# Kernel optimization log

Hardware: AMD Instinct MI355X
Metric: run time of the kernel (lower is better)

The kernel has to match this reference:

```python
import jax, jax.numpy as jnp
import numpy as np

B, C, H, W, NH = 8, 256, 32, 32, 4  # batch, channels, height, width, heads


def groupnorm(x, w, b, eps=1e-5):
    # GroupNorm with 1 group: normalize over (C,H,W) per sample
    mu = x.mean(axis=(1, 2, 3), keepdims=True)
    var = x.var(axis=(1, 2, 3), keepdims=True)
    xn = (x - mu) * jax.lax.rsqrt(var + eps)
    return xn * w[None, :, None, None] + b[None, :, None, None]


def setup_inputs() -> dict:
    key = jax.random.key(0)
    ks = jax.random.split(key, 6)
    C4 = 4 * C
    s = lambda k, shape, scale: jax.random.normal(k, shape, jnp.float32) * scale
    return {
        "x": jax.random.normal(ks[0], (B, C, H, W), jnp.float32),
        "qkv_w": s(ks[1], (3 * C, C), 0.05),   # 1x1 conv, no bias
        "uh_w": s(ks[2], (C, C), 0.05),
        "uh_b": jnp.zeros((C,), jnp.float32),
        "n1_w": jnp.ones((C,), jnp.float32),
        "n1_b": jnp.zeros((C,), jnp.float32),
        "n2_w": jnp.ones((C,), jnp.float32),
        "n2_b": jnp.zeros((C,), jnp.float32),
        "f1_w": s(ks[3], (C4, C), 0.05),
        "f1_b": jnp.zeros((C4,), jnp.float32),
        "f2_w": s(ks[4], (C, C4), 0.05),
        "f2_b": jnp.zeros((C,), jnp.float32),
        # torch inits these to 0; use nonzero values so both branches contribute
        "gamma_attn": jnp.array(0.5, jnp.float32),
        "gamma_ffn": jnp.array(0.5, jnp.float32),
    }


def reference(x, qkv_w, uh_w, uh_b, n1_w, n1_b, n2_w, n2_b,
              f1_w, f1_b, f2_w, f2_b, gamma_attn, gamma_ffn):
    Bx, Cx, Hx, Wx = x.shape
    N = Hx * Wx
    dk = Cx // NH
    # --- attention branch (eval mode: DropPath is identity) ---
    xn = groupnorm(x, n1_w, n1_b).reshape(Bx, Cx, N)
    qkv = jnp.einsum('oc,bcn->bon', qkv_w, xn)          # 1x1 conv == channel matmul
    q, k, v = [t.reshape(Bx, NH, dk, N) for t in jnp.split(qkv, 3, axis=1)]
    scores = jnp.einsum('bhdi,bhdj->bhij', q, k) / np.float32(np.sqrt(dk))
    attn = jax.nn.softmax(scores, axis=-1)               # [B,H,N,N]
    out = jnp.einsum('bhij,bhdj->bhdi', attn, v).reshape(Bx, Cx, N)
    uh = jnp.einsum('oc,bcn->bon', uh_w, out) + uh_b[None, :, None]
    x2 = x + gamma_attn * uh.reshape(Bx, Cx, Hx, Wx)
    # --- FFN branch ---
    h = groupnorm(x2, n2_w, n2_b).reshape(Bx, Cx, N)
    h = jax.nn.silu(jnp.einsum('oc,bcn->bon', f1_w, h) + f1_b[None, :, None])
    h = jnp.einsum('oc,bcn->bon', f2_w, h) + f2_b[None, :, None]
    return x2 + gamma_ffn * h.reshape(Bx, Cx, Hx, Wx)
```

## Files before the change

### kernel.cpp

```cpp
#include <hip/hip_runtime.h>
#include <math.h>

#define Bsz 8
#define Cch 256
#define Nsp 1024
#define NHd 4
#define QS  0.18033688011112042f

using bf16x8  = __attribute__((ext_vector_type(8))) short;
using f32x4   = __attribute__((ext_vector_type(4))) float;
using ushort8 = __attribute__((ext_vector_type(8))) unsigned short;
#define MFMA(a,b,c) __builtin_amdgcn_mfma_f32_16x16x32_bf16(a,b,c,0,0,0)

__device__ inline unsigned short f2bf(float f) {
    unsigned int u = __float_as_uint(f);
    u = u + 0x7fffu + ((u >> 16) & 1u);
    return (unsigned short)(u >> 16);
}
__device__ inline float bf2f(unsigned short u) {
    return __uint_as_float((unsigned int)u << 16);
}
__device__ inline unsigned int cvtpk(float lo, float hi) {
    unsigned int r;
    asm("v_cvt_pk_bf16_f32 %0, %1, %2" : "=v"(r) : "v"(lo), "v"(hi));
    return r;
}

__global__ __launch_bounds__(256) void wconv_gn(const float* __restrict__ a, const float* __restrict__ b,
                                                const float* __restrict__ c, const float* __restrict__ d,
                                                unsigned short* __restrict__ o,
                                                const float* __restrict__ x,
                                                float* __restrict__ part) {
    if (blockIdx.x < 3072) {
        size_t i = (size_t)blockIdx.x * 256 + threadIdx.x;
        float v;
        if (i < 196608) v = a[i];
        else if (i < 262144) v = b[i - 196608];
        else if (i < 524288) v = c[i - 262144];
        else v = d[i - 524288];
        o[i] = f2bf(v);
        return;
    }
    int blk = blockIdx.x - 3072;
    int bb = blk >> 6;
    const float* xb = x + (size_t)bb * (Cch * Nsp) + (size_t)(blk & 63) * 4096;
    int t = threadIdx.x;
    float s = 0.f, s2 = 0.f;
    for (int i = t; i < 4096; i += 256) { float v = xb[i]; s += v; s2 += v * v; }
    __shared__ float sh[256], sh2[256];
    sh[t] = s; sh2[t] = s2; __syncthreads();
    for (int off = 128; off; off >>= 1) {
        if (t < off) { sh[t] += sh[t + off]; sh2[t] += sh2[t + off]; }
        __syncthreads();
    }
    if (t == 0) { part[blk * 2] = sh[0]; part[blk * 2 + 1] = sh2[0]; }
}

template<int K, int KL, int NFRAG>
__global__ __launch_bounds__(256, 4) void gemm_lds(
        const unsigned short* __restrict__ W,
        const unsigned short* __restrict__ Xcl,
        int epi, int act, int xmode,
        unsigned short* __restrict__ ocl, int Ocl, int ocol0,
        unsigned short* __restrict__ orm,
        float* __restrict__ pf, const float* __restrict__ res,
        unsigned short* __restrict__ x2cl,
        const float* __restrict__ gamma, const float* __restrict__ bias,
        float* __restrict__ part,
        const float* __restrict__ gnpart,
        const float* __restrict__ gnw, const float* __restrict__ gnb) {
    static_assert(KL == 256 && K == 256, "single-round K only");
    constexpr int NTILE = NFRAG * 16;
    constexpr int CPR = KL / 8;
    constexpr int TOTCH = NTILE * CPR;
    int b = blockIdx.z, nb = blockIdx.x, ob = blockIdx.y;
    int t = threadIdx.x, w = t >> 6, l = t & 63, lg = l >> 4, lm = l & 15;
    __shared__ unsigned short Xs[NTILE * KL];
    __shared__ float sgn[2];
    const unsigned short* Xb = Xcl + ((size_t)b * Nsp + nb * NTILE) * K;
    int o_base = ob * 256 + w * 64;
    const unsigned short* Wp = W + (size_t)(o_base + lm) * K + 8 * lg;
    int m8 = lm & 15 & 7;

    bf16x8 wr[3][4];
    #define WLOAD(sl, g_) do {                                             \
        const unsigned short* wp_ = Wp + ((g_) & 7) * 32;                  \
        wr[sl][0] = *(const bf16x8*)(wp_);                                 \
        wr[sl][1] = *(const bf16x8*)(wp_ + (size_t)16 * K);                \
        wr[sl][2] = *(const bf16x8*)(wp_ + (size_t)32 * K);                \
        wr[sl][3] = *(const bf16x8*)(wp_ + (size_t)48 * K);                \
    } while (0)
    WLOAD(0, 0);
    WLOAD(1, 1);

    if (xmode == 0) {
        #pragma unroll
        for (int i = 0; i < TOTCH / 256; i++) {
            int c = i * 256 + t;
            int n = c / CPR, s = c % CPR;
            int gc = s ^ (n & 7);
            *(bf16x8*)&Xs[c * 8] = *(const bf16x8*)(Xb + (size_t)n * K + gc * 8);
        }
    } else if (xmode == 1) {
        if (t < 64) {
            float s = gnpart[(b * 64 + t) * 2], s2 = gnpart[(b * 64 + t) * 2 + 1];
            for (int m = 1; m < 64; m <<= 1) { s += __shfl_xor(s, m); s2 += __shfl_xor(s2, m); }
            if (t == 0) {
                float inv_n = 1.f / (Cch * Nsp);
                float mu = s * inv_n;
                float var = s2 * inv_n - mu * mu;
                sgn[0] = mu; sgn[1] = rsqrtf(var + 1e-5f);
            }
        }
        __syncthreads();
        float mu = sgn[0], rs = sgn[1];
        #pragma unroll
        for (int i = 0; i < TOTCH / 256; i++) {
            int c = i * 256 + t;
            int n = c / CPR, s = c % CPR;
            int gc = s ^ (n & 7);
            ushort8 xv = *(const ushort8*)(Xb + (size_t)n * K + gc * 8);
            f32x4 w0 = *(const f32x4*)(gnw + gc * 8);
            f32x4 w1 = *(const f32x4*)(gnw + gc * 8 + 4);
            f32x4 b0 = *(const f32x4*)(gnb + gc * 8);
            f32x4 b1 = *(const f32x4*)(gnb + gc * 8 + 4);
            ushort8 rr;
            #pragma unroll
            for (int j = 0; j < 4; j++) {
                rr[j]     = f2bf((bf2f(xv[j])     - mu) * rs * w0[j] + b0[j]);
                rr[4 + j] = f2bf((bf2f(xv[4 + j]) - mu) * rs * w1[j] + b1[j]);
            }
            *(ushort8*)&Xs[c * 8] = rr;
        }
    } else if (xmode == 2) {
        const size_t SPO = (size_t)Bsz * Nsp * Cch;
        #pragma unroll
        for (int i = 0; i < TOTCH / 256; i++) {
            int c = i * 256 + t;
            int n = c / CPR, s = c % CPR;
            int gc = s ^ (n & 7);
            const unsigned short* p0 = Xb + (size_t)n * K + gc * 8;
            int h = gc >> 3;
            int gn = nb * NTILE + n;
            float a0[8] = {};
            float lsum = 0.f;
            #pragma unroll
            for (int sp = 0; sp < 4; sp++) {
                ushort8 ov = *(const ushort8*)(p0 + (size_t)sp * SPO);
                #pragma unroll
                for (int j = 0; j < 8; j++) a0[j] += bf2f(ov[j]);
                lsum += gnpart[(((size_t)sp * Bsz + b) * NHd + h) * Nsp + gn];
            }
            float inv = 1.f / lsum;
            ushort8 rr;
            #pragma unroll
            for (int j = 0; j < 8; j++) rr[j] = f2bf(a0[j] * inv);
            *(ushort8*)&Xs[c * 8] = rr;
        }
    } else {
        if (t < 64) {
            float s = gnpart[(b * 64 + t) * 2], s2 = gnpart[(b * 64 + t) * 2 + 1];
            for (int m = 1; m < 64; m <<= 1) { s += __shfl_xor(s, m); s2 += __shfl_xor(s2, m); }
            if (t == 0) {
                float inv_n = 1.f / (Cch * Nsp);
                float mu = s * inv_n;
                float var = s2 * inv_n - mu * mu;
                sgn[0] = mu; sgn[1] = rsqrtf(var + 1e-5f);
            }
        }
        __syncthreads();
        float mu = sgn[0], rs = sgn[1];
        int n = t & 31;
        #pragma unroll
        for (int i = 0; i < 4; i++) {
            int G = i * 8 + (t >> 5);
            const float* xr = res + ((size_t)b * Cch + G * 8) * Nsp + (size_t)nb * NTILE + n;
            ushort8 rr;
            #pragma unroll
            for (int j = 0; j < 8; j++) {
                float val = xr[(size_t)j * Nsp];
                rr[j] = f2bf((val - mu) * rs * gnw[G * 8 + j] + gnb[G * 8 + j]);
            }
            int slot = G ^ (n & 7);
            *(ushort8*)&Xs[(n * 32 + slot) * 8] = rr;
        }
    }
    __syncthreads();

    f32x4 acc[4][NFRAG] = {};
    #define KSTEP(sl, s_) do {                                             \
        _Pragma("unroll")                                                  \
        for (int nf = 0; nf < NFRAG; nf++) {                               \
            int slot = ((s_) * 4 + lg) ^ m8;                               \
            bf16x8 xf = *(const bf16x8*)&Xs[((nf * 16 + lm) * CPR + slot) * 8]; \
            acc[0][nf] = MFMA(wr[sl][0], xf, acc[0][nf]);                  \
            acc[1][nf] = MFMA(wr[sl][1], xf, acc[1][nf]);                  \
            acc[2][nf] = MFMA(wr[sl][2], xf, acc[2][nf]);                  \
            acc[3][nf] = MFMA(wr[sl][3], xf, acc[3][nf]);                  \
        }                                                                  \
    } while (0)
    #pragma unroll
    for (int s = 0; s < 8; s++) {
        if (s < 6) WLOAD((s + 2) % 3, s + 2);
        KSTEP(s % 3, s);
    }
    #undef WLOAD
    #undef KSTEP

    if (epi == 0) {
        if (act == 3 && o_base >= 512) {
            #pragma unroll
            for (int nf = 0; nf < NFRAG; nf++) {
                int n = nb * NTILE + nf * 16 + lm;
                #pragma unroll
                for (int q = 0; q < 4; q++)
                    #pragma unroll
                    for (int r = 0; r < 4; r++) {
                        int o = o_base + q * 16 + 4 * lg + r - 512;
                        orm[((size_t)b * Cch + o) * Nsp + n] = f2bf(acc[q][nf][r]);
                    }
            }
        } else {
            float sc = (act == 3 && o_base < 256) ? QS : 1.f;
            #pragma unroll
            for (int nf = 0; nf < NFRAG; nf++) {
                int n = nb * NTILE + nf * 16 + lm;
                unsigned short* dst = ocl + ((size_t)b * Nsp + n) * Ocl + ocol0 + o_base + 4 * lg;
                #pragma unroll
                for (int q = 0; q < 4; q++) {
                    unsigned long long pk = 0;
                    #pragma unroll
                    for (int r = 0; r < 4; r++) {
                        int o = o_base + q * 16 + 4 * lg + r;
                        float v = acc[q][nf][r];
                        if (bias) v += bias[o];
                        if (act == 1) v = v / (1.f + __expf(-v));
                        else v *= sc;
                        pk |= (unsigned long long)f2bf(v) << (16 * r);
                    }
                    *(unsigned long long*)(dst + q * 16) = pk;
                }
            }
        }
    } else {
        float g = gamma[0];
        float ps = 0.f, ps2 = 0.f;
        #pragma unroll
        for (int nf = 0; nf < NFRAG; nf++) {
            int n = nb * NTILE + nf * 16 + lm;
            unsigned short* cdst = x2cl + ((size_t)b * Nsp + n) * Cch + o_base + 4 * lg;
            #pragma unroll
            for (int q = 0; q < 4; q++) {
                unsigned long long pk = 0;
                #pragma unroll
                for (int r = 0; r < 4; r++) {
                    int o = o_base + q * 16 + 4 * lg + r;
                    float v = acc[q][nf][r];
                    if (bias) v += bias[o];
                    size_t idx = ((size_t)b * Cch + o) * Nsp + n;
                    float ov = res[idx] + g * v;
                    pf[idx] = ov;
                    ps += ov; ps2 += ov * ov;
                    pk |= (unsigned long long)f2bf(ov) << (16 * r);
                }
                *(unsigned long long*)(cdst + q * 16) = pk;
            }
        }
        float* rsh  = (float*)&Xs[0];
        float* rsh2 = rsh + 256;
        __syncthreads();
        rsh[t] = ps; rsh2[t] = ps2; __syncthreads();
        for (int off = 128; off; off >>= 1) {
            if (t < off) { rsh[t] += rsh[t + off]; rsh2[t] += rsh2[t + off]; }
            __syncthreads();
        }
        if (t == 0) {
            int slot = b * gridDim.x + nb;
            part[slot * 2] = rsh[0]; part[slot * 2 + 1] = rsh2[0];
        }
    }
}

__global__ __launch_bounds__(256, 2) void ffn_fused(
        const unsigned short* __restrict__ Wf1,
        const unsigned short* __restrict__ Wf2,
        const unsigned short* __restrict__ x2cl,
        const float* __restrict__ gnpart,
        const float* __restrict__ gnw, const float* __restrict__ gnb,
        const float* __restrict__ f1b, const float* __restrict__ f2b,
        const float* __restrict__ gamma,
        const float* __restrict__ x2, float* __restrict__ out) {
    int b = blockIdx.z, nb = blockIdx.x;
    int t = threadIdx.x, w = t >> 6, l = t & 63, lg = l >> 4, lm = l & 15;
    __shared__ unsigned short Xs[32 * 256];
    __shared__ unsigned short H[4][32 * 256];
    __shared__ float sgn[2];
    const unsigned short* Xb = x2cl + ((size_t)b * Nsp + nb * 32) * 256;
    int m8 = lm & 7;

    bf16x8 wr[3][4];
    const unsigned short* Wp;
    #define WLOADF(sl, g_, KK) do {                                        \
        const unsigned short* wp_ = Wp + ((g_) >> 3) * 256 + ((g_) & 7) * 32; \
        wr[sl][0] = *(const bf16x8*)(wp_);                                 \
        wr[sl][1] = *(const bf16x8*)(wp_ + (size_t)16 * (KK));             \
        wr[sl][2] = *(const bf16x8*)(wp_ + (size_t)32 * (KK));             \
        wr[sl][3] = *(const bf16x8*)(wp_ + (size_t)48 * (KK));             \
    } while (0)

    if (t < 64) {
        float s = gnpart[(b * 64 + t) * 2], s2 = gnpart[(b * 64 + t) * 2 + 1];
        for (int m = 1; m < 64; m <<= 1) { s += __shfl_xor(s, m); s2 += __shfl_xor(s2, m); }
        if (t == 0) {
            float inv_n = 1.f / (Cch * Nsp);
            float mu = s * inv_n;
            float var = s2 * inv_n - mu * mu;
            sgn[0] = mu; sgn[1] = rsqrtf(var + 1e-5f);
        }
    }
    Wp = Wf1 + (size_t)(w * 64 + lm) * 256 + 8 * lg;
    WLOADF(0, 0, 256);
    WLOADF(1, 1, 256);
    __syncthreads();
    {
        float mu = sgn[0], rs = sgn[1];
        #pragma unroll
        for (int i = 0; i < 4; i++) {
            int c = i * 256 + t;
            int n = c / 32, s = c % 32;
            int gc = s ^ (n & 7);
            ushort8 xv = *(const ushort8*)(Xb + (size_t)n * 256 + gc * 8);
            f32x4 w0 = *(const f32x4*)(gnw + gc * 8);
            f32x4 w1 = *(const f32x4*)(gnw + gc * 8 + 4);
            f32x4 b0 = *(const f32x4*)(gnb + gc * 8);
            f32x4 b1 = *(const f32x4*)(gnb + gc * 8 + 4);
            ushort8 rr;
            #pragma unroll
            for (int j = 0; j < 4; j++) {
                rr[j]     = f2bf((bf2f(xv[j])     - mu) * rs * w0[j] + b0[j]);
                rr[4 + j] = f2bf((bf2f(xv[4 + j]) - mu) * rs * w1[j] + b1[j]);
            }
            *(ushort8*)&Xs[c * 8] = rr;
        }
    }
    __syncthreads();

    f32x4 acc[4][2];
    #define KSTEPF(sl, s_, Xp) do {                                        \
        _Pragma("unroll")                                                  \
        for (int nf = 0; nf < 2; nf++) {                                   \
            int slot = ((s_) * 4 + lg) ^ m8;                               \
            bf16x8 xf = *(const bf16x8*)&(Xp)[((nf * 16 + lm) * 32 + slot) * 8]; \
            acc[0][nf] = MFMA(wr[sl][0], xf, acc[0][nf]);                  \
            acc[1][nf] = MFMA(wr[sl][1], xf, acc[1][nf]);                  \
            acc[2][nf] = MFMA(wr[sl][2], xf, acc[2][nf]);                  \
            acc[3][nf] = MFMA(wr[sl][3], xf, acc[3][nf]);                  \
        }                                                                  \
    } while (0)
    #define F1PASS(obp, NEXTPROLOG) do {                                   \
        _Pragma("unroll")                                                  \
        for (int q = 0; q < 4; q++)                                        \
            _Pragma("unroll")                                              \
            for (int nf = 0; nf < 2; nf++) acc[q][nf] = (f32x4){0.f, 0.f, 0.f, 0.f}; \
        _Pragma("unroll")                                                  \
        for (int s = 0; s < 8; s++) {                                      \
            if (s < 6) WLOADF((s + 2) % 3, s + 2, 256);                    \
            KSTEPF(s % 3, s, Xs);                                          \
        }                                                                  \
        NEXTPROLOG;                                                        \
        _Pragma("unroll")                                                  \
        for (int nf = 0; nf < 2; nf++) {                                   \
            int n = nf * 16 + lm;                                          \
            _Pragma("unroll")                                              \
            for (int q = 0; q < 4; q++) {                                  \
                unsigned long long pk = 0;                                 \
                _Pragma("unroll")                                          \
                for (int r = 0; r < 4; r++) {                              \
                    int oin = w * 64 + q * 16 + 4 * lg + r;                \
                    float v = acc[q][nf][r] + f1b[(obp) * 256 + oin];      \
                    v = v / (1.f + __expf(-v));                            \
                    pk |= (unsigned long long)f2bf(v) << (16 * r);         \
                }                                                          \
                int G = w * 8 + q * 2 + (lg >> 1);                         \
                int slot = G ^ (n & 7);                                    \
                *(unsigned long long*)&H[obp][(n * 32 + slot) * 8 + 4 * (lg & 1)] = pk; \
            }                                                              \
        }                                                                  \
    } while (0)

    F1PASS(0, { Wp = Wf1 + (size_t)(256 + w * 64 + lm) * 256 + 8 * lg;
                WLOADF(0, 0, 256); WLOADF(1, 1, 256); });
    F1PASS(1, { Wp = Wf1 + (size_t)(512 + w * 64 + lm) * 256 + 8 * lg;
                WLOADF(0, 0, 256); WLOADF(1, 1, 256); });
    F1PASS(2, { Wp = Wf1 + (size_t)(768 + w * 64 + lm) * 256 + 8 * lg;
                WLOADF(0, 0, 256); WLOADF(1, 1, 256); });
    F1PASS(3, { Wp = Wf2 + (size_t)(w * 64 + lm) * 1024 + 8 * lg;
                WLOADF(0, 0, 1024); WLOADF(1, 1, 1024); });
    __syncthreads();

    #pragma unroll
    for (int q = 0; q < 4; q++)
        #pragma unroll
        for (int nf = 0; nf < 2; nf++) acc[q][nf] = (f32x4){0.f, 0.f, 0.f, 0.f};
    #pragma unroll
    for (int g = 0; g < 32; g++) {
        if (g < 30) WLOADF((g + 2) % 3, g + 2, 1024);
        KSTEPF(g % 3, g & 7, H[g >> 3]);
    }
    #undef WLOADF
    #undef KSTEPF
    #undef F1PASS

    float gm = gamma[0];
    #pragma unroll
    for (int nf = 0; nf < 2; nf++) {
        int n = nb * 32 + nf * 16 + lm;
        #pragma unroll
        for (int q = 0; q < 4; q++) {
            #pragma unroll
            for (int r = 0; r < 4; r++) {
                int o = w * 64 + q * 16 + 4 * lg + r;
                size_t idx = ((size_t)b * Cch + o) * Nsp + n;
                out[idx] = x2[idx] + gm * (acc[q][nf][r] + f2b[o]);
            }
        }
    }
}

__global__ __launch_bounds__(256) void attn_mfma8(const unsigned short* __restrict__ qk,
                                                  const unsigned short* __restrict__ v,
                                                  unsigned short* __restrict__ Opart,
                                                  float* __restrict__ lpart) {
    int L = blockIdx.x;
    int xcd = L & 7, jj = L >> 3;
    int g = xcd * 4 + (jj >> 5);
    int m = jj & 31;
    int h = g & 3, b = g >> 2;
    int ib = m & 7, sp = m >> 3;
    int t = threadIdx.x, w = t >> 6, l = t & 63, lg = l >> 4, lm = l & 15;
    __shared__ unsigned short KVs[2][4096];
    __shared__ unsigned short P[4][2][32][36];
    int i0 = ib * 128 + w * 32;
    int j0 = sp * 256;
    const unsigned short* qb = qk + ((size_t)b * Nsp + i0 + lm) * 512 + h * 64 + 8 * lg;
    bf16x8 qf00 = *(const bf16x8*)(qb);
    bf16x8 qf01 = *(const bf16x8*)(qb + 32);
    bf16x8 qf10 = *(const bf16x8*)(qb + 16 * 512);
    bf16x8 qf11 = *(const bf16x8*)(qb + 16 * 512 + 32);

    const unsigned short *gs0, *gs1;
    int lo0, lo1;
    size_t gstep;
    if (t < 128) {
        int c = 2 * t;
        int r = c >> 3, s = c & 7, swr = r & 7;
        const unsigned short* rowp = qk + ((size_t)b * Nsp + j0 + r) * 512 + 256 + h * 64;
        gs0 = rowp + ((s ^ swr) * 8);
        gs1 = rowp + (((s + 1) ^ swr) * 8);
        lo0 = c * 8; lo1 = lo0 + 8;
        gstep = (size_t)32 * 512;
    } else {
        int c = 2 * (t - 128);
        int d = c >> 2, s = c & 3, swd = d & 3;
        const unsigned short* rowp = v + ((size_t)b * Cch + h * 64 + d) * Nsp + j0;
        gs0 = rowp + ((s ^ swd) * 8);
        gs1 = rowp + (((s + 1) ^ swd) * 8);
        lo0 = 2048 + c * 8; lo1 = lo0 + 8;
        gstep = 32;
    }
    int cA = (lg ^ (lm & 7)) * 8;
    int cB = ((4 + lg) ^ (lm & 7)) * 8;
    int cV = (lg ^ (lm & 3)) * 8;

    f32x4 O00 = {}, O01 = {}, O02 = {}, O03 = {};
    f32x4 O10 = {}, O11 = {}, O12 = {}, O13 = {};
    float ls0 = 0.f, ls1 = 0.f;
    bf16x8 sg0, sg1;

    #define ISSUE(tile) do { sg0 = *(const bf16x8*)(gs0 + (size_t)(tile) * gstep); \
                             sg1 = *(const bf16x8*)(gs1 + (size_t)(tile) * gstep); } while (0)
    #define WRITE(bu) do { *(bf16x8*)&KVs[bu][lo0] = sg0; \
                           *(bf16x8*)&KVs[bu][lo1] = sg1; } while (0)
    #define QKC8(bu, pb) do {                                                     \
        const unsigned short* Ka = KVs[bu] + lm * 64;                             \
        const unsigned short* Kc = KVs[bu] + (16 + lm) * 64;                      \
        bf16x8 k00 = *(const bf16x8*)(Ka + cA);                                   \
        bf16x8 k01 = *(const bf16x8*)(Ka + cB);                                   \
        bf16x8 k10 = *(const bf16x8*)(Kc + cA);                                   \
        bf16x8 k11 = *(const bf16x8*)(Kc + cB);                                   \
        f32x4 s00 = {}, s01 = {}, s10 = {}, s11 = {};                             \
        s00 = MFMA(k00, qf00, s00); s00 = MFMA(k01, qf01, s00);                   \
        s01 = MFMA(k00, qf10, s01); s01 = MFMA(k01, qf11, s01);                   \
        s10 = MFMA(k10, qf00, s10); s10 = MFMA(k11, qf01, s10);                   \
        s11 = MFMA(k10, qf10, s11); s11 = MFMA(k11, qf11, s11);                   \
        float p0, p1, p2, p3; uint2 pk;                                           \
        p0 = exp2f(s00[0]); p1 = exp2f(s00[1]); p2 = exp2f(s00[2]); p3 = exp2f(s00[3]); \
        ls0 += (p0 + p1) + (p2 + p3);                                             \
        pk.x = cvtpk(p0, p1); pk.y = cvtpk(p2, p3);                               \
        *(uint2*)&P[w][pb][lm][4 * lg] = pk;                                      \
        p0 = exp2f(s01[0]); p1 = exp2f(s01[1]); p2 = exp2f(s01[2]); p3 = exp2f(s01[3]); \
        ls1 += (p0 + p1) + (p2 + p3);                                             \
        pk.x = cvtpk(p0, p1); pk.y = cvtpk(p2, p3);                               \
        *(uint2*)&P[w][pb][16 + lm][4 * lg] = pk;                                 \
        p0 = exp2f(s10[0]); p1 = exp2f(s10[1]); p2 = exp2f(s10[2]); p3 = exp2f(s10[3]); \
        ls0 += (p0 + p1) + (p2 + p3);                                             \
        pk.x = cvtpk(p0, p1); pk.y = cvtpk(p2, p3);                               \
        *(uint2*)&P[w][pb][lm][16 + 4 * lg] = pk;                                 \
        p0 = exp2f(s11[0]); p1 = exp2f(s11[1]); p2 = exp2f(s11[2]); p3 = exp2f(s11[3]); \
        ls1 += (p0 + p1) + (p2 + p3);                                             \
        pk.x = cvtpk(p0, p1); pk.y = cvtpk(p2, p3);                               \
        *(uint2*)&P[w][pb][16 + lm][16 + 4 * lg] = pk;                            \
    } while (0)
    #define PVC8(bu, pb) do {                                                     \
        bf16x8 pa0 = *(const bf16x8*)&P[w][pb][lm][8 * lg];                       \
        bf16x8 pa1 = *(const bf16x8*)&P[w][pb][16 + lm][8 * lg];                  \
        const unsigned short* Vl = KVs[bu] + 2048;                                \
        bf16x8 v0 = *(const bf16x8*)(Vl + lm * 32 + cV);                          \
        bf16x8 v1 = *(const bf16x8*)(Vl + (16 + lm) * 32 + cV);                   \
        bf16x8 v2 = *(const bf16x8*)(Vl + (32 + lm) * 32 + cV);                   \
        bf16x8 v3 = *(const bf16x8*)(Vl + (48 + lm) * 32 + cV);                   \
        O00 = MFMA(v0, pa0, O00); O10 = MFMA(v0, pa1, O10);                       \
        O01 = MFMA(v1, pa0, O01); O11 = MFMA(v1, pa1, O11);                       \
        O02 = MFMA(v2, pa0, O02); O12 = MFMA(v2, pa1, O12);                       \
        O03 = MFMA(v3, pa0, O03); O13 = MFMA(v3, pa1, O13);                       \
    } while (0)

    ISSUE(0); WRITE(0); __syncthreads();
    ISSUE(1);
    QKC8(0, 0);
    __syncthreads();
    WRITE(1);
    __syncthreads();
    #pragma unroll
    for (int tt = 1; tt < 8; tt++) {
        if (tt < 7) ISSUE(tt + 1);
        QKC8(tt & 1, tt & 1);
        PVC8((tt - 1) & 1, (tt - 1) & 1);
        __syncthreads();
        if (tt < 7) WRITE((tt + 1) & 1);
        __syncthreads();
    }
    PVC8(1, 1);
    #undef ISSUE
    #undef WRITE
    #undef QKC8
    #undef PVC8

    ls0 += __shfl_xor(ls0, 16); ls0 += __shfl_xor(ls0, 32);
    ls1 += __shfl_xor(ls1, 16); ls1 += __shfl_xor(ls1, 32);
    if (lg == 0) {
        float* lp = lpart + (((size_t)sp * Bsz + b) * NHd + h) * Nsp + i0 + lm;
        lp[0] = ls0;
        lp[16] = ls1;
    }
    unsigned short* ob0 = Opart + (((size_t)sp * Bsz + b) * Nsp + i0 + lm) * Cch + h * 64 + 4 * lg;
    unsigned short* ob1 = ob0 + (size_t)16 * Cch;
    uint2 pk;
    #define STO(dt, Oa, Ob_) \
        pk.x = cvtpk(Oa[0], Oa[1]); pk.y = cvtpk(Oa[2], Oa[3]); \
        *(uint2*)(ob0 + dt * 16) = pk; \
        pk.x = cvtpk(Ob_[0], Ob_[1]); pk.y = cvtpk(Ob_[2], Ob_[3]); \
        *(uint2*)(ob1 + dt * 16) = pk;
    STO(0, O00, O10) STO(1, O01, O11) STO(2, O02, O12) STO(3, O03, O13)
    #undef STO
}

extern "C" void kernel_launch(void* const* d_in, const int* in_sizes, int n_in,
                              void* d_out, int out_size, void* d_ws, size_t ws_size,
                              hipStream_t stream) {
    const float* x      = (const float*)d_in[0];
    const float* qkv_w  = (const float*)d_in[1];
    const float* uh_w   = (const float*)d_in[2];
    const float* uh_b   = (const float*)d_in[3];
    const float* n1_w   = (const float*)d_in[4];
    const float* n1_b   = (const float*)d_in[5];
    const float* n2_w   = (const float*)d_in[6];
    const float* n2_b   = (const float*)d_in[7];
    const float* f1_w   = (const float*)d_in[8];
    const float* f1_b   = (const float*)d_in[9];
    const float* f2_w   = (const float*)d_in[10];
    const float* f2_b   = (const float*)d_in[11];
    const float* g_attn = (const float*)d_in[12];
    const float* g_ffn  = (const float*)d_in[13];
    float* out = (float*)d_out;
    char* ws = (char*)d_ws;

    float*          part1   = (float*)(ws + 1024);
    float*          part2   = (float*)(ws + 5120);
    unsigned short* wbf     = (unsigned short*)(ws + 16384);
    float*          lpart   = (float*)(ws + 2097152);
    unsigned short* qk_cl   = (unsigned short*)(ws + 6291456);
    unsigned short* vbuf    = (unsigned short*)(ws + 14680064);
    unsigned short* x2cl    = (unsigned short*)(ws + 14680064);
    unsigned short* Opart   = (unsigned short*)(ws + 23068672);
    float*          x2      = (float*)(ws + 50331648);

    unsigned short* wbf_qkv = wbf;
    unsigned short* wbf_uh  = wbf + 196608;
    unsigned short* wbf_f1  = wbf + 262144;
    unsigned short* wbf_f2  = wbf + 524288;

    wconv_gn<<<3584, 256, 0, stream>>>(qkv_w, uh_w, f1_w, f2_w, wbf, x, part1);

    gemm_lds<256, 256, 2><<<dim3(32, 3, Bsz), 256, 0, stream>>>(wbf_qkv,
        (const unsigned short*)x, 0, 3, 3,
        qk_cl, 512, 0, vbuf, nullptr, x, nullptr, nullptr, nullptr, nullptr,
        part1, n1_w, n1_b);
    attn_mfma8<<<1024, 256, 0, stream>>>(qk_cl, vbuf, Opart, lpart);
    gemm_lds<256, 256, 1><<<dim3(64, 1, Bsz), 256, 0, stream>>>(wbf_uh, Opart, 2, 0, 2,
        nullptr, 0, 0, nullptr, x2, x, x2cl, g_attn, uh_b, part2,
        lpart, nullptr, nullptr);

    ffn_fused<<<dim3(32, 1, Bsz), 256, 0, stream>>>(wbf_f1, wbf_f2, x2cl,
        part2, n2_w, n2_b, f1_b, f2_b, g_ffn, x2, out);
}
```

Measured before the change: 113.4 us.

## Run fused FFN kernel with eight waves and split work across wave groups

The fused FFN kernel moves from 256 to 512 threads per block. Two wave groups each compute half of the F1 output channels per pass, so there are two passes instead of four. In the F2 stage each of the eight waves owns 32 output channels instead of 64. The register-array weight pipeline is also replaced with named registers in explicit rotation, in both the GEMM and FFN kernels. The aim is more latency hiding per block on the FFN stage, at the cost of higher register and occupancy pressure with the 512,2 launch bounds.

```diff
diff --git a/kernel.cpp b/kernel.cpp
--- a/kernel.cpp
+++ b/kernel.cpp
@@ -80,18 +80,17 @@
     const unsigned short* Xb = Xcl + ((size_t)b * Nsp + nb * NTILE) * K;
     int o_base = ob * 256 + w * 64;
     const unsigned short* Wp = W + (size_t)(o_base + lm) * K + 8 * lg;
-    int m8 = lm & 15 & 7;
-
-    bf16x8 wr[3][4];
-    #define WLOAD(sl, g_) do {                                             \
-        const unsigned short* wp_ = Wp + ((g_) & 7) * 32;                  \
-        wr[sl][0] = *(const bf16x8*)(wp_);                                 \
-        wr[sl][1] = *(const bf16x8*)(wp_ + (size_t)16 * K);                \
-        wr[sl][2] = *(const bf16x8*)(wp_ + (size_t)32 * K);                \
-        wr[sl][3] = *(const bf16x8*)(wp_ + (size_t)48 * K);                \
-    } while (0)
-    WLOAD(0, 0);
-    WLOAD(1, 1);
+    int m8 = lm & 7;
+
+    bf16x8 wA0, wA1, wA2, wA3, wB0, wB1, wB2, wB3, wC0, wC1, wC2, wC3;
+    #define WL(d0, d1, d2, d3, ks_) do {                                   \
+        d0 = *(const bf16x8*)(Wp + (size_t)(0)      + (ks_) * 32);         \
+        d1 = *(const bf16x8*)(Wp + (size_t)16 * K   + (ks_) * 32);         \
+        d2 = *(const bf16x8*)(Wp + (size_t)32 * K   + (ks_) * 32);         \
+        d3 = *(const bf16x8*)(Wp + (size_t)48 * K   + (ks_) * 32);         \
+    } while (0)
+    WL(wA0, wA1, wA2, wA3, 0);
+    WL(wB0, wB1, wB2, wB3, 1);
 
     if (xmode == 0) {
         #pragma unroll
@@ -188,24 +187,27 @@
     __syncthreads();
 
     f32x4 acc[4][NFRAG] = {};
-    #define KSTEP(sl, s_) do {                                             \
+    #define KS(w0_, w1_, w2_, w3_, ks_) do {                               \
         _Pragma("unroll")                                                  \
         for (int nf = 0; nf < NFRAG; nf++) {                               \
-            int slot = ((s_) * 4 + lg) ^ m8;                               \
+            int slot = ((ks_) * 4 + lg) ^ m8;                              \
             bf16x8 xf = *(const bf16x8*)&Xs[((nf * 16 + lm) * CPR + slot) * 8]; \
-            acc[0][nf] = MFMA(wr[sl][0], xf, acc[0][nf]);                  \
-            acc[1][nf] = MFMA(wr[sl][1], xf, acc[1][nf]);                  \
-            acc[2][nf] = MFMA(wr[sl][2], xf, acc[2][nf]);                  \
-            acc[3][nf] = MFMA(wr[sl][3], xf, acc[3][nf]);                  \
+            acc[0][nf] = MFMA(w0_, xf, acc[0][nf]);                        \
+            acc[1][nf] = MFMA(w1_, xf, acc[1][nf]);                        \
+            acc[2][nf] = MFMA(w2_, xf, acc[2][nf]);                        \
+            acc[3][nf] = MFMA(w3_, xf, acc[3][nf]);                        \
         }                                                                  \
     } while (0)
-    #pragma unroll
-    for (int s = 0; s < 8; s++) {
-        if (s < 6) WLOAD((s + 2) % 3, s + 2);
-        KSTEP(s % 3, s);
-    }
-    #undef WLOAD
-    #undef KSTEP
+    WL(wC0, wC1, wC2, wC3, 2); KS(wA0, wA1, wA2, wA3, 0);
+    WL(wA0, wA1, wA2, wA3, 3); KS(wB0, wB1, wB2, wB3, 1);
+    WL(wB0, wB1, wB2, wB3, 4); KS(wC0, wC1, wC2, wC3, 2);
+    WL(wC0, wC1, wC2, wC3, 5); KS(wA0, wA1, wA2, wA3, 3);
+    WL(wA0, wA1, wA2, wA3, 6); KS(wB0, wB1, wB2, wB3, 4);
+    WL(wB0, wB1, wB2, wB3, 7); KS(wC0, wC1, wC2, wC3, 5);
+    KS(wA0, wA1, wA2, wA3, 6);
+    KS(wB0, wB1, wB2, wB3, 7);
+    #undef WL
+    #undef KS
 
     if (epi == 0) {
         if (act == 3 && o_base >= 512) {
@@ -281,7 +283,7 @@
     }
 }
 
-__global__ __launch_bounds__(256, 2) void ffn_fused(
+__global__ __launch_bounds__(512, 2) void ffn_fused(
         const unsigned short* __restrict__ Wf1,
         const unsigned short* __restrict__ Wf2,
         const unsigned short* __restrict__ x2cl,
@@ -292,20 +294,20 @@
         const float* __restrict__ x2, float* __restrict__ out) {
     int b = blockIdx.z, nb = blockIdx.x;
     int t = threadIdx.x, w = t >> 6, l = t & 63, lg = l >> 4, lm = l & 15;
+    int wq = w >> 2, wr = w & 3;
     __shared__ unsigned short Xs[32 * 256];
     __shared__ unsigned short H[4][32 * 256];
     __shared__ float sgn[2];
     const unsigned short* Xb = x2cl + ((size_t)b * Nsp + nb * 32) * 256;
     int m8 = lm & 7;
 
-    bf16x8 wr[3][4];
+    bf16x8 wA0, wA1, wA2, wA3, wB0, wB1, wB2, wB3, wC0, wC1, wC2, wC3;
     const unsigned short* Wp;
-    #define WLOADF(sl, g_, KK) do {                                        \
-        const unsigned short* wp_ = Wp + ((g_) >> 3) * 256 + ((g_) & 7) * 32; \
-        wr[sl][0] = *(const bf16x8*)(wp_);                                 \
-        wr[sl][1] = *(const bf16x8*)(wp_ + (size_t)16 * (KK));             \
-        wr[sl][2] = *(const bf16x8*)(wp_ + (size_t)32 * (KK));             \
-        wr[sl][3] = *(const bf16x8*)(wp_ + (size_t)48 * (KK));             \
+    #define WL1(d0, d1, d2, d3, ks_) do {                                  \
+        d0 = *(const bf16x8*)(Wp + (ks_) * 32);                            \
+        d1 = *(const bf16x8*)(Wp + (size_t)16 * 256 + (ks_) * 32);         \
+        d2 = *(const bf16x8*)(Wp + (size_t)32 * 256 + (ks_) * 32);         \
+        d3 = *(const bf16x8*)(Wp + (size_t)48 * 256 + (ks_) * 32);         \
     } while (0)
 
     if (t < 64) {
@@ -318,16 +320,16 @@
             sgn[0] = mu; sgn[1] = rsqrtf(var + 1e-5f);
         }
     }
-    Wp = Wf1 + (size_t)(w * 64 + lm) * 256 + 8 * lg;
-    WLOADF(0, 0, 256);
-    WLOADF(1, 1, 256);
+    Wp = Wf1 + (size_t)(wq * 256 + wr * 64 + lm) * 256 + 8 * lg;
+    WL1(wA0, wA1, wA2, wA3, 0);
+    WL1(wB0, wB1, wB2, wB3, 1);
     __syncthreads();
     {
         float mu = sgn[0], rs = sgn[1];
         #pragma unroll
-        for (int i = 0; i < 4; i++) {
-            int c = i * 256 + t;
-            int n = c / 32, s = c % 32;
+        for (int i = 0; i < 2; i++) {
+            int c = i * 512 + t;
+            int n = c >> 5, s = c & 31;
             int gc = s ^ (n & 7);
             ushort8 xv = *(const ushort8*)(Xb + (size_t)n * 256 + gc * 8);
             f32x4 w0 = *(const f32x4*)(gnw + gc * 8);
@@ -346,28 +348,29 @@
     __syncthreads();
 
     f32x4 acc[4][2];
-    #define KSTEPF(sl, s_, Xp) do {                                        \
+    #define KS1(w0_, w1_, w2_, w3_, ks_) do {                              \
         _Pragma("unroll")                                                  \
         for (int nf = 0; nf < 2; nf++) {                                   \
-            int slot = ((s_) * 4 + lg) ^ m8;                               \
-            bf16x8 xf = *(const bf16x8*)&(Xp)[((nf * 16 + lm) * 32 + slot) * 8]; \
-            acc[0][nf] = MFMA(wr[sl][0], xf, acc[0][nf]);                  \
-            acc[1][nf] = MFMA(wr[sl][1], xf, acc[1][nf]);                  \
-            acc[2][nf] = MFMA(wr[sl][2], xf, acc[2][nf]);                  \
-            acc[3][nf] = MFMA(wr[sl][3], xf, acc[3][nf]);                  \
+            int slot = ((ks_) * 4 + lg) ^ m8;                              \
+            bf16x8 xf = *(const bf16x8*)&Xs[((nf * 16 + lm) * 32 + slot) * 8]; \
+            acc[0][nf] = MFMA(w0_, xf, acc[0][nf]);                        \
+            acc[1][nf] = MFMA(w1_, xf, acc[1][nf]);                        \
+            acc[2][nf] = MFMA(w2_, xf, acc[2][nf]);                        \
+            acc[3][nf] = MFMA(w3_, xf, acc[3][nf]);                        \
         }                                                                  \
     } while (0)
-    #define F1PASS(obp, NEXTPROLOG) do {                                   \
-        _Pragma("unroll")                                                  \
-        for (int q = 0; q < 4; q++)                                        \
-            _Pragma("unroll")                                              \
-            for (int nf = 0; nf < 2; nf++) acc[q][nf] = (f32x4){0.f, 0.f, 0.f, 0.f}; \
-        _Pragma("unroll")                                                  \
-        for (int s = 0; s < 8; s++) {                                      \
-            if (s < 6) WLOADF((s + 2) % 3, s + 2, 256);                    \
-            KSTEPF(s % 3, s, Xs);                                          \
-        }                                                                  \
-        NEXTPROLOG;                                                        \
+    #define F1CHAIN() do {                                                 \
+        WL1(wC0, wC1, wC2, wC3, 2); KS1(wA0, wA1, wA2, wA3, 0);            \
+        WL1(wA0, wA1, wA2, wA3, 3); KS1(wB0, wB1, wB2, wB3, 1);            \
+        WL1(wB0, wB1, wB2, wB3, 4); KS1(wC0, wC1, wC2, wC3, 2);            \
+        WL1(wC0, wC1, wC2, wC3, 5); KS1(wA0, wA1, wA2, wA3, 3);            \
+        WL1(wA0, wA1, wA2, wA3, 6); KS1(wB0, wB1, wB2, wB3, 4);            \
+        WL1(wB0, wB1, wB2, wB3, 7); KS1(wC0, wC1, wC2, wC3, 5);            \
+        KS1(wA0, wA1, wA2, wA3, 6);                                        \
+        KS1(wB0, wB1, wB2, wB3, 7);                                        \
+    } while (0)
+    #define F1EPI(p_) do {                                                 \
+        int hb = (p_) * 2 + wq;                                            \
         _Pragma("unroll")                                                  \
         for (int nf = 0; nf < 2; nf++) {                                   \
             int n = nf * 16 + lm;                                          \
@@ -376,52 +379,105 @@
                 unsigned long long pk = 0;                                 \
                 _Pragma("unroll")                                          \
                 for (int r = 0; r < 4; r++) {                              \
-                    int oin = w * 64 + q * 16 + 4 * lg + r;                \
-                    float v = acc[q][nf][r] + f1b[(obp) * 256 + oin];      \
+                    int oin = wr * 64 + q * 16 + 4 * lg + r;               \
+                    float v = acc[q][nf][r] + f1b[(p_) * 512 + wq * 256 + oin]; \
                     v = v / (1.f + __expf(-v));                            \
                     pk |= (unsigned long long)f2bf(v) << (16 * r);         \
                 }                                                          \
-                int G = w * 8 + q * 2 + (lg >> 1);                         \
+                int G = wr * 8 + q * 2 + (lg >> 1);                        \
                 int slot = G ^ (n & 7);                                    \
-                *(unsigned long long*)&H[obp][(n * 32 + slot) * 8 + 4 * (lg & 1)] = pk; \
+                *(unsigned long long*)&H[hb][(n * 32 + slot) * 8 + 4 * (lg & 1)] = pk; \
             }                                                              \
         }                                                                  \
     } while (0)
 
-    F1PASS(0, { Wp = Wf1 + (size_t)(256 + w * 64 + lm) * 256 + 8 * lg;
-                WLOADF(0, 0, 256); WLOADF(1, 1, 256); });
-    F1PASS(1, { Wp = Wf1 + (size_t)(512 + w * 64 + lm) * 256 + 8 * lg;
-                WLOADF(0, 0, 256); WLOADF(1, 1, 256); });
-    F1PASS(2, { Wp = Wf1 + (size_t)(768 + w * 64 + lm) * 256 + 8 * lg;
-                WLOADF(0, 0, 256); WLOADF(1, 1, 256); });
-    F1PASS(3, { Wp = Wf2 + (size_t)(w * 64 + lm) * 1024 + 8 * lg;
-                WLOADF(0, 0, 1024); WLOADF(1, 1, 1024); });
-    __syncthreads();
-
     #pragma unroll
     for (int q = 0; q < 4; q++)
         #pragma unroll
         for (int nf = 0; nf < 2; nf++) acc[q][nf] = (f32x4){0.f, 0.f, 0.f, 0.f};
+    F1CHAIN();
+    Wp = Wf1 + (size_t)(512 + wq * 256 + wr * 64 + lm) * 256 + 8 * lg;
+    WL1(wA0, wA1, wA2, wA3, 0);
+    WL1(wB0, wB1, wB2, wB3, 1);
+    F1EPI(0);
     #pragma unroll
-    for (int g = 0; g < 32; g++) {
-        if (g < 30) WLOADF((g + 2) % 3, g + 2, 1024);
-        KSTEPF(g % 3, g & 7, H[g >> 3]);
-    }
-    #undef WLOADF
-    #undef KSTEPF
-    #undef F1PASS
+    for (int q = 0; q < 4; q++)
+        #pragma unroll
+        for (int nf = 0; nf < 2; nf++) acc[q][nf] = (f32x4){0.f, 0.f, 0.f, 0.f};
+    F1CHAIN();
+    #undef WL1
+    #undef KS1
+    #undef F1CHAIN
+
+    const unsigned short* Wp2 = Wf2 + (size_t)(w * 32 + lm) * 1024 + 8 * lg;
+    bf16x8 u0, u1, v0, v1, z0, z1;
+    #define WL2(d0, d1, ks_) do {                                          \
+        d0 = *(const bf16x8*)(Wp2 + (ks_) * 32);                           \
+        d1 = *(const bf16x8*)(Wp2 + (size_t)16 * 1024 + (ks_) * 32);       \
+    } while (0)
+    WL2(u0, u1, 0);
+    WL2(v0, v1, 1);
+    F1EPI(1);
+    #undef F1EPI
+    __syncthreads();
+
+    f32x4 ac2[2][2] = {};
+    #define KS2(e0, e1, g_) do {                                           \
+        int slot = (((g_) & 7) * 4 + lg) ^ m8;                             \
+        const unsigned short* Hp = H[(g_) >> 3];                           \
+        _Pragma("unroll")                                                  \
+        for (int nf = 0; nf < 2; nf++) {                                   \
+            bf16x8 xf = *(const bf16x8*)&Hp[((nf * 16 + lm) * 32 + slot) * 8]; \
+            ac2[0][nf] = MFMA(e0, xf, ac2[0][nf]);                         \
+            ac2[1][nf] = MFMA(e1, xf, ac2[1][nf]);                         \
+        }                                                                  \
+    } while (0)
+    WL2(z0, z1, 2);  KS2(u0, u1, 0);
+    WL2(u0, u1, 3);  KS2(v0, v1, 1);
+    WL2(v0, v1, 4);  KS2(z0, z1, 2);
+    WL2(z0, z1, 5);  KS2(u0, u1, 3);
+    WL2(u0, u1, 6);  KS2(v0, v1, 4);
+    WL2(v0, v1, 7);  KS2(z0, z1, 5);
+    WL2(z0, z1, 8);  KS2(u0, u1, 6);
+    WL2(u0, u1, 9);  KS2(v0, v1, 7);
+    WL2(v0, v1, 10); KS2(z0, z1, 8);
+    WL2(z0, z1, 11); KS2(u0, u1, 9);
+    WL2(u0, u1, 12); KS2(v0, v1, 10);
+    WL2(v0, v1, 13); KS2(z0, z1, 11);
+    WL2(z0, z1, 14); KS2(u0, u1, 12);
+    WL2(u0, u1, 15); KS2(v0, v1, 13);
+    WL2(v0, v1, 16); KS2(z0, z1, 14);
+    WL2(z0, z1, 17); KS2(u0, u1, 15);
+    WL2(u0, u1, 18); KS2(v0, v1, 16);
+    WL2(v0, v1, 19); KS2(z0, z1, 17);
+    WL2(z0, z1, 20); KS2(u0, u1, 18);
+    WL2(u0, u1, 21); KS2(v0, v1, 19);
+    WL2(v0, v1, 22); KS2(z0, z1, 20);
+    WL2(z0, z1, 23); KS2(u0, u1, 21);
+    WL2(u0, u1, 24); KS2(v0, v1, 22);
+    WL2(v0, v1, 25); KS2(z0, z1, 23);
+    WL2(z0, z1, 26); KS2(u0, u1, 24);
+    WL2(u0, u1, 27); KS2(v0, v1, 25);
+    WL2(v0, v1, 28); KS2(z0, z1, 26);
+    WL2(z0, z1, 29); KS2(u0, u1, 27);
+    WL2(u0, u1, 30); KS2(v0, v1, 28);
+    WL2(v0, v1, 31); KS2(z0, z1, 29);
+    KS2(u0, u1, 30);
+    KS2(v0, v1, 31);
+    #undef WL2
+    #undef KS2
 
     float gm = gamma[0];
     #pragma unroll
     for (int nf = 0; nf < 2; nf++) {
         int n = nb * 32 + nf * 16 + lm;
         #pragma unroll
-        for (int q = 0; q < 4; q++) {
+        for (int ch = 0; ch < 2; ch++) {
             #pragma unroll
             for (int r = 0; r < 4; r++) {
-                int o = w * 64 + q * 16 + 4 * lg + r;
+                int o = w * 32 + ch * 16 + 4 * lg + r;
                 size_t idx = ((size_t)b * Cch + o) * Nsp + n;
-                out[idx] = x2[idx] + gm * (acc[q][nf][r] + f2b[o]);
+                out[idx] = x2[idx] + gm * (ac2[ch][nf][r] + f2b[o]);
             }
         }
     }
@@ -611,6 +667,6 @@
         nullptr, 0, 0, nullptr, x2, x, x2cl, g_attn, uh_b, part2,
         lpart, nullptr, nullptr);
 
-    ffn_fused<<<dim3(32, 1, Bsz), 256, 0, stream>>>(wbf_f1, wbf_f2, x2cl,
+    ffn_fused<<<dim3(32, 1, Bsz), 512, 0, stream>>>(wbf_f1, wbf_f2, x2cl,
         part2, n2_w, n2_b, f1_b, f2_b, g_ffn, x2, out);
 }
```

Measured after the change: 106.0 us. 1.07x faster.
